# Performance work log

Measured on AMD Instinct MI355X. Metric: run time of the kernel, lower is better.

## Reference

```python
import jax, jax.numpy as jnp
import numpy as np

SIGMA, U = 16.0, 0.0
B, C, L, H = 4, 2048, 96, 8   # L = n_head windows, H = d_k window width
D = L * H                      # d_model = 768
D_INNER = 3072


def make_gauss_mask():
    # replicates My_EncoderLayer.gauss: guass_2d[j, k] = g[(L-1-j) + k]
    x = jnp.arange(-L, L, dtype=jnp.float32)
    g = jnp.exp(-(x - U) ** 2 / (2.0 * SIGMA ** 2))
    g = g / jnp.max(g)
    idx = (L - 1) - jnp.arange(L)[:, None] + jnp.arange(L)[None, :]
    return g[idx]  # (L, L)


def layer_norm(x, g, b, eps=1e-6):
    m = jnp.mean(x, axis=-1, keepdims=True)
    v = jnp.var(x, axis=-1, keepdims=True)
    return (x - m) / jnp.sqrt(v + eps) * g + b


def setup_inputs() -> dict:
    key = jax.random.key(0)
    ks = jax.random.split(key, 16)
    sH = 1.0 / np.sqrt(H)
    sD = 1.0 / np.sqrt(D)
    sI = 1.0 / np.sqrt(D_INNER)
    n = lambda k, shape, s: jax.random.normal(k, shape, jnp.float32) * s
    return {
        "enc_input": jax.random.normal(ks[0], (B, C, D), jnp.float32),
        "mask": make_gauss_mask(),
        "w_q": n(ks[1], (H,), sH), "b_q": n(ks[2], (), sH),
        "w_k": n(ks[3], (H,), sH), "b_k": n(ks[4], (), sH),
        "w_v": n(ks[5], (H,), sH), "b_v": n(ks[6], (), sH),
        "ln1_g": jnp.ones((D,), jnp.float32), "ln1_b": jnp.zeros((D,), jnp.float32),
        "w1": n(ks[7], (D, D_INNER), sD), "b1": n(ks[8], (D_INNER,), sD),
        "w2": n(ks[9], (D_INNER, D), sI), "b2": n(ks[10], (D,), sI),
        "ln2_g": jnp.ones((D,), jnp.float32), "ln2_b": jnp.zeros((D,), jnp.float32),
    }


def reference(enc_input, mask, w_q, b_q, w_k, b_k, w_v, b_v,
              ln1_g, ln1_b, w1, b1, w2, b2, ln2_g, ln2_b):
    Bn, Cn, Dm = enc_input.shape
    Ln = mask.shape[0]
    Hn = Dm // Ln
    heads = enc_input.reshape(Bn, Cn, Ln, Hn)              # unfold(-1, H, H)
    q = jnp.einsum('bclh,h->bcl', heads, w_q) + b_q        # (B,C,L)
    k = jnp.einsum('bclh,h->bcl', heads, w_k) + b_k
    v = jnp.einsum('bclh,h->bcl', heads, w_v) + b_v
    fm = q[..., :, None] * k[..., None, :]                 # outer product (B,C,L,L)
    nrm = jnp.sqrt(jnp.sum(fm * fm, axis=(2, 3), keepdims=True))  # F.normalize over flat L*L
    fm = fm / jnp.maximum(nrm, 1e-12)
    scores = jnp.sum(fm * mask, axis=-1)                   # gaussian-masked sum -> (B,C,L)
    attn = jax.nn.softmax(scores, axis=-1)
    res = attn * v                                         # (B,C,L)
    x = (res[..., None] + heads).reshape(Bn, Cn, Dm)       # broadcast add residual
    x = layer_norm(x, ln1_g, ln1_b)
    # PositionwiseFeedForward: w2(relu(w1(x))) + residual, then LN
    h = jax.nn.relu(jnp.einsum('bcd,df->bcf', x, w1) + b1)
    y = jnp.einsum('bcf,fd->bcd', h, w2) + b2 + x
    return layer_norm(y, ln2_g, ln2_b)
```

## Files before the change

### kernel.cpp

```cpp
#include <hip/hip_runtime.h>

#define ROWS 8192
#define LW 96
#define HW 8
#define DM 768
#define DI 3072

typedef __bf16 bf16x8 __attribute__((ext_vector_type(8)));
typedef float f32x4 __attribute__((ext_vector_type(4)));
typedef unsigned short u16;
typedef unsigned int u32;

__device__ __forceinline__ u16 bfbits(__bf16 b) {
    return __builtin_bit_cast(u16, b);
}
__device__ __forceinline__ void decomp(float v, u16& hi, u16& lo) {
    __bf16 hb = (__bf16)v;
    float hf = (float)hb;
    __bf16 lb = (__bf16)(v - hf);
    hi = bfbits(hb); lo = bfbits(lb);
}
__device__ __forceinline__ void gload16(const void* g, void* l) {
    __builtin_amdgcn_global_load_lds((const __attribute__((address_space(1))) unsigned int*)g,
                                     (__attribute__((address_space(3))) unsigned int*)l, 16, 0, 0);
}
__device__ __forceinline__ float wred_sum(float v) {
#pragma unroll
    for (int o = 32; o; o >>= 1) v += __shfl_xor(v, o);
    return v;
}
__device__ __forceinline__ float wred_max(float v) {
#pragma unroll
    for (int o = 32; o; o >>= 1) v = fmaxf(v, __shfl_xor(v, o));
    return v;
}

__global__ __launch_bounds__(256) void k_wprep(
    const float* __restrict__ W, u16* __restrict__ Th,
    u16* __restrict__ Tl, int K, int N)
{
    __shared__ float tile[32][33];
    const int tx = threadIdx.x & 31, ty = threadIdx.x >> 5;
    const int k0 = blockIdx.y * 32, n0 = blockIdx.x * 32;
#pragma unroll
    for (int i = 0; i < 32; i += 8)
        tile[ty + i][tx] = W[(size_t)(k0 + ty + i) * N + n0 + tx];
    __syncthreads();
#pragma unroll
    for (int i = 0; i < 32; i += 8) {
        int n = n0 + ty + i, k = k0 + tx;
        u16 h, l;
        decomp(tile[tx][ty + i], h, l);
        Th[(size_t)n * K + k] = h;
        Tl[(size_t)n * K + k] = l;
    }
}

__global__ __launch_bounds__(256) void k_attn_ln1(
    const float* __restrict__ inp, const float* __restrict__ mask,
    const float* __restrict__ wq, const float* __restrict__ bq,
    const float* __restrict__ wk, const float* __restrict__ bk,
    const float* __restrict__ wv, const float* __restrict__ bv,
    const float* __restrict__ g1, const float* __restrict__ be1,
    float* __restrict__ xout, u16* __restrict__ xh)
{
    const int t = threadIdx.x, lane = t & 63, w = t >> 6;
    const int row = blockIdx.x * 4 + w;
    __shared__ float kvS[4][96];
    __shared__ float gS[4][192];

    const float* rp = inp + (size_t)row * DM;

    float xr[8], xr2[8];
    {
        float4 a = ((const float4*)rp)[lane * 2];
        float4 b = ((const float4*)rp)[lane * 2 + 1];
        xr[0]=a.x; xr[1]=a.y; xr[2]=a.z; xr[3]=a.w;
        xr[4]=b.x; xr[5]=b.y; xr[6]=b.z; xr[7]=b.w;
    }
    if (lane < 32) {
        float4 a = ((const float4*)rp)[128 + lane * 2];
        float4 b = ((const float4*)rp)[128 + lane * 2 + 1];
        xr2[0]=a.x; xr2[1]=a.y; xr2[2]=a.z; xr2[3]=a.w;
        xr2[4]=b.x; xr2[5]=b.y; xr2[6]=b.z; xr2[7]=b.w;
    } else {
#pragma unroll
        for (int i = 0; i < 8; i++) xr2[i] = 0.f;
    }

    {
        int m1 = lane;
        gS[w][m1] = mask[95 * LW + m1];
        int m2 = 64 + lane;
        gS[w][m2] = (m2 < 96) ? mask[95 * LW + m2] : mask[(190 - m2) * LW + 95];
        int m3 = 128 + lane;
        if (m3 <= 190) gS[w][m3] = mask[(190 - m3) * LW + 95];
    }

    float q1, k1, v1, q2, k2, v2;
    {
        float aq = 0.f, ak = 0.f, av = 0.f, aq2 = 0.f, ak2 = 0.f, av2 = 0.f;
#pragma unroll
        for (int i = 0; i < 8; i++) {
            float wqi = wq[i], wki = wk[i], wvi = wv[i];
            aq = fmaf(xr[i],  wqi, aq);  ak = fmaf(xr[i],  wki, ak);  av = fmaf(xr[i],  wvi, av);
            aq2 = fmaf(xr2[i], wqi, aq2); ak2 = fmaf(xr2[i], wki, ak2); av2 = fmaf(xr2[i], wvi, av2);
        }
        q1 = aq + bq[0]; k1 = ak + bk[0]; v1 = av + bv[0];
        q2 = aq2 + bq[0]; k2 = ak2 + bk[0]; v2 = av2 + bv[0];
    }

    kvS[w][lane] = k1;
    if (lane < 32) kvS[w][64 + lane] = k2;
    asm volatile("s_waitcnt lgkmcnt(0)" ::: "memory");

    float nq2 = wred_sum(q1 * q1 + (lane < 32 ? q2 * q2 : 0.f));
    float nk2 = wred_sum(k1 * k1 + (lane < 32 ? k2 * k2 : 0.f));
    float inv = 1.f / fmaxf(sqrtf(nq2) * sqrtf(nk2), 1e-12f);

    float km1 = 0.f, km2 = 0.f;
    {
        const float* gw = gS[w];
        const float* kw = kvS[w];
        const int b1 = 95 - lane;
        const int b2 = (lane < 32) ? (31 - lane) : 0;
#pragma unroll 4
        for (int kk = 0; kk < 96; kk++) {
            float kv = kw[kk];
            km1 = fmaf(gw[b1 + kk], kv, km1);
            km2 = fmaf(gw[b2 + kk], kv, km2);
        }
    }

    float sc1 = q1 * km1 * inv;
    float sc2 = (lane < 32) ? (q2 * km2 * inv) : -1e30f;
    float mx = wred_max(fmaxf(sc1, sc2));
    float e1 = __expf(sc1 - mx);
    float e2 = (lane < 32) ? __expf(sc2 - mx) : 0.f;
    float se = wred_sum(e1 + e2);
    float r1 = (e1 / se) * v1;
    float r2 = (e2 / se) * v2;

    float xn[8], xn2[8];
    float sum = 0.f;
#pragma unroll
    for (int i = 0; i < 8; i++) { xn[i] = xr[i] + r1; sum += xn[i]; }
    if (lane < 32) {
#pragma unroll
        for (int i = 0; i < 8; i++) { xn2[i] = xr2[i] + r2; sum += xn2[i]; }
    }
    float mean = wred_sum(sum) * (1.f / DM);
    float vs = 0.f;
#pragma unroll
    for (int i = 0; i < 8; i++) { float d = xn[i] - mean; vs += d * d; }
    if (lane < 32) {
#pragma unroll
        for (int i = 0; i < 8; i++) { float d = xn2[i] - mean; vs += d * d; }
    }
    float rstd = rsqrtf(wred_sum(vs) * (1.f / DM) + 1e-6f);

    float* xo = xout + (size_t)row * DM;
    u16* xho = xh + (size_t)row * DM;
    {
        const int d0 = lane * 8;
        float4 ga = ((const float4*)(g1 + d0))[0], gb = ((const float4*)(g1 + d0))[1];
        float4 ba = ((const float4*)(be1 + d0))[0], bb = ((const float4*)(be1 + d0))[1];
        float o[8];
        o[0]=(xn[0]-mean)*rstd*ga.x+ba.x; o[1]=(xn[1]-mean)*rstd*ga.y+ba.y;
        o[2]=(xn[2]-mean)*rstd*ga.z+ba.z; o[3]=(xn[3]-mean)*rstd*ga.w+ba.w;
        o[4]=(xn[4]-mean)*rstd*gb.x+bb.x; o[5]=(xn[5]-mean)*rstd*gb.y+bb.y;
        o[6]=(xn[6]-mean)*rstd*gb.z+bb.z; o[7]=(xn[7]-mean)*rstd*gb.w+bb.w;
        ((float4*)(xo + d0))[0] = make_float4(o[0], o[1], o[2], o[3]);
        ((float4*)(xo + d0))[1] = make_float4(o[4], o[5], o[6], o[7]);
        uint4 pk;
        pk.x = (u32)bfbits((__bf16)o[0]) | ((u32)bfbits((__bf16)o[1]) << 16);
        pk.y = (u32)bfbits((__bf16)o[2]) | ((u32)bfbits((__bf16)o[3]) << 16);
        pk.z = (u32)bfbits((__bf16)o[4]) | ((u32)bfbits((__bf16)o[5]) << 16);
        pk.w = (u32)bfbits((__bf16)o[6]) | ((u32)bfbits((__bf16)o[7]) << 16);
        *(uint4*)(xho + d0) = pk;
    }
    if (lane < 32) {
        const int d0 = 512 + lane * 8;
        float4 ga = ((const float4*)(g1 + d0))[0], gb = ((const float4*)(g1 + d0))[1];
        float4 ba = ((const float4*)(be1 + d0))[0], bb = ((const float4*)(be1 + d0))[1];
        float o[8];
        o[0]=(xn2[0]-mean)*rstd*ga.x+ba.x; o[1]=(xn2[1]-mean)*rstd*ga.y+ba.y;
        o[2]=(xn2[2]-mean)*rstd*ga.z+ba.z; o[3]=(xn2[3]-mean)*rstd*ga.w+ba.w;
        o[4]=(xn2[4]-mean)*rstd*gb.x+bb.x; o[5]=(xn2[5]-mean)*rstd*gb.y+bb.y;
        o[6]=(xn2[6]-mean)*rstd*gb.z+bb.z; o[7]=(xn2[7]-mean)*rstd*gb.w+bb.w;
        ((float4*)(xo + d0))[0] = make_float4(o[0], o[1], o[2], o[3]);
        ((float4*)(xo + d0))[1] = make_float4(o[4], o[5], o[6], o[7]);
        uint4 pk;
        pk.x = (u32)bfbits((__bf16)o[0]) | ((u32)bfbits((__bf16)o[1]) << 16);
        pk.y = (u32)bfbits((__bf16)o[2]) | ((u32)bfbits((__bf16)o[3]) << 16);
        pk.z = (u32)bfbits((__bf16)o[4]) | ((u32)bfbits((__bf16)o[5]) << 16);
        pk.w = (u32)bfbits((__bf16)o[6]) | ((u32)bfbits((__bf16)o[7]) << 16);
        *(uint4*)(xho + d0) = pk;
    }
}

template<int SPLITK, int RELU, int OUT_MODE>
__global__ __launch_bounds__(256, 3) void k_gemm4(
    const u16* __restrict__ Ah,
    const u16* __restrict__ Bh, const u16* __restrict__ Bl,
    const float* __restrict__ bias, float* __restrict__ Cf,
    u16* __restrict__ Ch, int M, int N, int K)
{
    __shared__ u16 S[2 * 12288];

    const int t = threadIdx.x;
    const int lane = t & 63, w = t >> 6;
    const int wm = w >> 1, wn = w & 1;
    const int fr = lane & 15, fq = lane >> 4;

    const int gn = gridDim.x, gm = gridDim.y;
    int Lidx = blockIdx.x + gn * (blockIdx.y + gm * blockIdx.z);
    const int nb = gn * gm * SPLITK;
    int sID = ((nb & 7) == 0) ? ((Lidx & 7) * (nb >> 3) + (Lidx >> 3)) : Lidx;
    const int bz = sID / (gn * gm);
    const int rr = sID - bz * (gn * gm);
    const int bm = rr / gn;
    const int bn = rr - bm * gn;

    const int KS = K / SPLITK;
    const int NT = KS / 32;
    const int kb = bz * KS;

    const int r0 = t >> 2;
    const int c0 = (t & 3) ^ ((r0 >> 1) & 3);
    const size_t aoff  = (size_t)(bm * 128 + r0) * K + kb + c0 * 8;
    const size_t aoff2 = aoff + (size_t)64 * K;
    const size_t boff  = (size_t)(bn * 128 + r0) * K + kb + c0 * 8;
    const size_t boff2 = boff + (size_t)64 * K;
    const int w512 = w * 512;

    f32x4 acc[4][4];
#pragma unroll
    for (int i = 0; i < 4; i++)
#pragma unroll
        for (int j = 0; j < 4; j++) acc[i][j] = (f32x4)0.f;

    int ai[4], bi[4];
#pragma unroll
    for (int i = 0; i < 4; i++) { int rA = wm * 64 + i * 16 + fr; ai[i] = rA * 32 + (fq ^ ((rA >> 1) & 3)) * 8; }
#pragma unroll
    for (int j = 0; j < 4; j++) { int rB = wn * 64 + j * 16 + fr; bi[j] = rB * 32 + (fq ^ ((rB >> 1) & 3)) * 8; }

#define STAGE(tile, bb)                                                  \
    { u16* Lb = S + (bb) * 12288 + w512;                                 \
      const size_t kk = (size_t)(tile) * 32;                             \
      gload16(Ah + aoff  + kk, Lb + 0);                                  \
      gload16(Ah + aoff2 + kk, Lb + 2048);                               \
      gload16(Bh + boff  + kk, Lb + 4096);                               \
      gload16(Bh + boff2 + kk, Lb + 6144);                               \
      gload16(Bl + boff  + kk, Lb + 8192);                               \
      gload16(Bl + boff2 + kk, Lb + 10240); }

#define MM(ii, jj, AA, BH, BL)                                                            \
    acc[ii][jj] = __builtin_amdgcn_mfma_f32_16x16x32_bf16(AA, BH, acc[ii][jj], 0, 0, 0);  \
    acc[ii][jj] = __builtin_amdgcn_mfma_f32_16x16x32_bf16(AA, BL, acc[ii][jj], 0, 0, 0);

    STAGE(0, 0);

    for (int tt = 0; tt < NT; ++tt) {
        if (tt + 1 < NT) {
            STAGE(tt + 1, (tt + 1) & 1);
            asm volatile("s_waitcnt vmcnt(6)" ::: "memory");
        } else {
            asm volatile("s_waitcnt vmcnt(0)" ::: "memory");
        }
        __builtin_amdgcn_s_barrier();

        const u16* Lp = S + (tt & 1) * 12288;
        bf16x8 a[4], bh[4], bl[4];
#pragma unroll
        for (int j = 0; j < 4; j++) {
            bh[j] = *(const bf16x8*)&Lp[4096 + bi[j]];
            bl[j] = *(const bf16x8*)&Lp[8192 + bi[j]];
        }
#pragma unroll
        for (int i = 0; i < 4; i++) a[i] = *(const bf16x8*)&Lp[ai[i]];

        __builtin_amdgcn_s_setprio(1);
#pragma unroll
        for (int j = 0; j < 4; j++)
#pragma unroll
            for (int i = 0; i < 4; i++) { MM(i, j, a[i], bh[j], bl[j]) }
        __builtin_amdgcn_s_setprio(0);

        __builtin_amdgcn_s_barrier();
    }
#undef STAGE
#undef MM

    float* Cp = (OUT_MODE == 1) ? (Cf + (size_t)bz * M * N) : Cf;
#pragma unroll
    for (int i = 0; i < 4; i++) {
        const int row = bm * 128 + wm * 64 + i * 16 + fq * 4;
#pragma unroll
        for (int j = 0; j < 4; j++) {
            const int col = bn * 128 + wn * 64 + j * 16 + fr;
            if (OUT_MODE == 0) {
                const float bb = bias[col];
#pragma unroll
                for (int rg = 0; rg < 4; rg++) {
                    size_t off = (size_t)(row + rg) * N + col;
                    float v = acc[i][j][rg] + bb;
                    if (RELU) v = fmaxf(v, 0.f);
                    Ch[off] = bfbits((__bf16)v);
                }
            } else {
#pragma unroll
                for (int rg = 0; rg < 4; rg++) {
                    size_t off = (size_t)(row + rg) * N + col;
                    Cp[off] = acc[i][j][rg];
                }
            }
        }
    }
}

__global__ __launch_bounds__(256) void k_ln2f(
    const float* __restrict__ y0, const float* __restrict__ y1,
    const float* __restrict__ x, const float* __restrict__ b2,
    const float* __restrict__ g, const float* __restrict__ b,
    float* __restrict__ out)
{
    const int t = threadIdx.x, lane = t & 63, w = t >> 6;
    const int row = blockIdx.x * 4 + w;
    const size_t base = (size_t)row * DM + lane * 12;

    float xs[12]; float sum = 0.f;
#pragma unroll
    for (int i = 0; i < 3; i++) {
        float4 a = ((const float4*)(y0 + base))[i];
        float4 bv = ((const float4*)(y1 + base))[i];
        float4 c = ((const float4*)(x + base))[i];
        float4 d = ((const float4*)(b2 + lane * 12))[i];
        xs[i*4+0] = a.x + bv.x + c.x + d.x;
        xs[i*4+1] = a.y + bv.y + c.y + d.y;
        xs[i*4+2] = a.z + bv.z + c.z + d.z;
        xs[i*4+3] = a.w + bv.w + c.w + d.w;
        sum += xs[i*4+0] + xs[i*4+1] + xs[i*4+2] + xs[i*4+3];
    }
    float mean = wred_sum(sum) * (1.f / DM);
    float vs = 0.f;
#pragma unroll
    for (int i = 0; i < 12; i++) { float dd = xs[i] - mean; vs += dd * dd; }
    float rstd = rsqrtf(wred_sum(vs) * (1.f / DM) + 1e-6f);
#pragma unroll
    for (int i = 0; i < 3; i++) {
        float4 gv = ((const float4*)(g + lane * 12))[i];
        float4 bb = ((const float4*)(b + lane * 12))[i];
        float4 o;
        o.x = (xs[i*4+0] - mean) * rstd * gv.x + bb.x;
        o.y = (xs[i*4+1] - mean) * rstd * gv.y + bb.y;
        o.z = (xs[i*4+2] - mean) * rstd * gv.z + bb.z;
        o.w = (xs[i*4+3] - mean) * rstd * gv.w + bb.w;
        ((float4*)(out + base))[i] = o;
    }
}

extern "C" void kernel_launch(void* const* d_in, const int* in_sizes, int n_in,
                              void* d_out, int out_size, void* d_ws, size_t ws_size,
                              hipStream_t stream) {
    const float* enc  = (const float*)d_in[0];
    const float* mask = (const float*)d_in[1];
    const float* wq = (const float*)d_in[2];  const float* bq = (const float*)d_in[3];
    const float* wk = (const float*)d_in[4];  const float* bk = (const float*)d_in[5];
    const float* wv = (const float*)d_in[6];  const float* bv = (const float*)d_in[7];
    const float* g1 = (const float*)d_in[8];  const float* be1 = (const float*)d_in[9];
    const float* w1 = (const float*)d_in[10]; const float* b1  = (const float*)d_in[11];
    const float* w2 = (const float*)d_in[12]; const float* b2  = (const float*)d_in[13];
    const float* g2 = (const float*)d_in[14]; const float* be2 = (const float*)d_in[15];
    float* out = (float*)d_out;

    char* p = (char*)d_ws;
    float* x  = (float*)p;                 p += (size_t)ROWS * DM * 4;
    float* y01 = (float*)p;                p += 2 * (size_t)ROWS * DM * 4;
    u16* xh = (u16*)p; p += (size_t)ROWS * DM * 2;
    u16* hh = (u16*)p; p += (size_t)ROWS * DI * 2;
    u16* w1h = (u16*)p; p += (size_t)DM * DI * 2;
    u16* w1l = (u16*)p; p += (size_t)DM * DI * 2;
    u16* w2h = (u16*)p; p += (size_t)DM * DI * 2;
    u16* w2l = (u16*)p; p += (size_t)DM * DI * 2;

    k_wprep<<<dim3(DI / 32, DM / 32), 256, 0, stream>>>(w1, w1h, w1l, DM, DI);
    k_wprep<<<dim3(DM / 32, DI / 32), 256, 0, stream>>>(w2, w2h, w2l, DI, DM);

    k_attn_ln1<<<ROWS / 4, 256, 0, stream>>>(enc, mask, wq, bq, wk, bk, wv, bv, g1, be1,
                                             x, xh);

    k_gemm4<1, 1, 0><<<dim3(DI / 128, ROWS / 128, 1), 256, 0, stream>>>(
        xh, w1h, w1l, b1, nullptr, hh, ROWS, DI, DM);

    k_gemm4<2, 0, 1><<<dim3(DM / 128, ROWS / 128, 2), 256, 0, stream>>>(
        hh, w2h, w2l, nullptr, y01, nullptr, ROWS, DM, DI);

    k_ln2f<<<ROWS / 4, 256, 0, stream>>>(y01, y01 + (size_t)ROWS * DM, x, b2, g2, be2, out);
}
```

Before: 316.2 us.

## Switch GEMMs from split bf16 hi/lo weights to single fp16 MFMA

The bf16 hi+lo weight decomposition, which needed two MFMAs per tile and twice the B-operand loads, is replaced by one fp16 copy of each weight and a single fp16 MFMA. Activations are also stored as fp16. LDS per block shrinks, so the occupancy hint goes from 3 to 4 blocks. A block-index remap that walks M fastest is added for the first GEMM. This halves matrix-core work and weight traffic, at the cost of fp16 precision on weights, which risks accuracy loss or overflow for large activations.

After: 255.7 us. 19.2% less time.

```diff
diff --git a/kernel.cpp b/kernel.cpp
--- a/kernel.cpp
+++ b/kernel.cpp
@@ -6,19 +6,15 @@
 #define DM 768
 #define DI 3072
 
-typedef __bf16 bf16x8 __attribute__((ext_vector_type(8)));
+typedef _Float16 f16;
+typedef f16 f16x8 __attribute__((ext_vector_type(8)));
 typedef float f32x4 __attribute__((ext_vector_type(4)));
 typedef unsigned short u16;
 typedef unsigned int u32;
 
-__device__ __forceinline__ u16 bfbits(__bf16 b) {
-    return __builtin_bit_cast(u16, b);
-}
-__device__ __forceinline__ void decomp(float v, u16& hi, u16& lo) {
-    __bf16 hb = (__bf16)v;
-    float hf = (float)hb;
-    __bf16 lb = (__bf16)(v - hf);
-    hi = bfbits(hb); lo = bfbits(lb);
+__device__ __forceinline__ u16 f16bits(float v) {
+    f16 h = (f16)v;
+    return __builtin_bit_cast(u16, h);
 }
 __device__ __forceinline__ void gload16(const void* g, void* l) {
     __builtin_amdgcn_global_load_lds((const __attribute__((address_space(1))) unsigned int*)g,
@@ -36,8 +32,7 @@
 }
 
 __global__ __launch_bounds__(256) void k_wprep(
-    const float* __restrict__ W, u16* __restrict__ Th,
-    u16* __restrict__ Tl, int K, int N)
+    const float* __restrict__ W, u16* __restrict__ Th, int K, int N)
 {
     __shared__ float tile[32][33];
     const int tx = threadIdx.x & 31, ty = threadIdx.x >> 5;
@@ -49,10 +44,7 @@
 #pragma unroll
     for (int i = 0; i < 32; i += 8) {
         int n = n0 + ty + i, k = k0 + tx;
-        u16 h, l;
-        decomp(tile[tx][ty + i], h, l);
-        Th[(size_t)n * K + k] = h;
-        Tl[(size_t)n * K + k] = l;
+        Th[(size_t)n * K + k] = f16bits(tile[tx][ty + i]);
     }
 }
 
@@ -173,10 +165,10 @@
         ((float4*)(xo + d0))[0] = make_float4(o[0], o[1], o[2], o[3]);
         ((float4*)(xo + d0))[1] = make_float4(o[4], o[5], o[6], o[7]);
         uint4 pk;
-        pk.x = (u32)bfbits((__bf16)o[0]) | ((u32)bfbits((__bf16)o[1]) << 16);
-        pk.y = (u32)bfbits((__bf16)o[2]) | ((u32)bfbits((__bf16)o[3]) << 16);
-        pk.z = (u32)bfbits((__bf16)o[4]) | ((u32)bfbits((__bf16)o[5]) << 16);
-        pk.w = (u32)bfbits((__bf16)o[6]) | ((u32)bfbits((__bf16)o[7]) << 16);
+        pk.x = (u32)f16bits(o[0]) | ((u32)f16bits(o[1]) << 16);
+        pk.y = (u32)f16bits(o[2]) | ((u32)f16bits(o[3]) << 16);
+        pk.z = (u32)f16bits(o[4]) | ((u32)f16bits(o[5]) << 16);
+        pk.w = (u32)f16bits(o[6]) | ((u32)f16bits(o[7]) << 16);
         *(uint4*)(xho + d0) = pk;
     }
     if (lane < 32) {
@@ -191,22 +183,21 @@
         ((float4*)(xo + d0))[0] = make_float4(o[0], o[1], o[2], o[3]);
         ((float4*)(xo + d0))[1] = make_float4(o[4], o[5], o[6], o[7]);
         uint4 pk;
-        pk.x = (u32)bfbits((__bf16)o[0]) | ((u32)bfbits((__bf16)o[1]) << 16);
-        pk.y = (u32)bfbits((__bf16)o[2]) | ((u32)bfbits((__bf16)o[3]) << 16);
-        pk.z = (u32)bfbits((__bf16)o[4]) | ((u32)bfbits((__bf16)o[5]) << 16);
-        pk.w = (u32)bfbits((__bf16)o[6]) | ((u32)bfbits((__bf16)o[7]) << 16);
+        pk.x = (u32)f16bits(o[0]) | ((u32)f16bits(o[1]) << 16);
+        pk.y = (u32)f16bits(o[2]) | ((u32)f16bits(o[3]) << 16);
+        pk.z = (u32)f16bits(o[4]) | ((u32)f16bits(o[5]) << 16);
+        pk.w = (u32)f16bits(o[6]) | ((u32)f16bits(o[7]) << 16);
         *(uint4*)(xho + d0) = pk;
     }
 }
 
-template<int SPLITK, int RELU, int OUT_MODE>
-__global__ __launch_bounds__(256, 3) void k_gemm4(
-    const u16* __restrict__ Ah,
-    const u16* __restrict__ Bh, const u16* __restrict__ Bl,
+template<int SPLITK, int RELU, int OUT_MODE, int BMFAST>
+__global__ __launch_bounds__(256, 4) void k_gemm4(
+    const u16* __restrict__ Ah, const u16* __restrict__ Bh,
     const float* __restrict__ bias, float* __restrict__ Cf,
     u16* __restrict__ Ch, int M, int N, int K)
 {
-    __shared__ u16 S[2 * 12288];
+    __shared__ u16 S[2 * 8192];
 
     const int t = threadIdx.x;
     const int lane = t & 63, w = t >> 6;
@@ -219,8 +210,9 @@
     int sID = ((nb & 7) == 0) ? ((Lidx & 7) * (nb >> 3) + (Lidx >> 3)) : Lidx;
     const int bz = sID / (gn * gm);
     const int rr = sID - bz * (gn * gm);
-    const int bm = rr / gn;
-    const int bn = rr - bm * gn;
+    int bm, bn;
+    if (BMFAST) { bm = rr % gm; bn = rr / gm; }
+    else        { bm = rr / gn; bn = rr - (rr / gn) * gn; }
 
     const int KS = K / SPLITK;
     const int NT = KS / 32;
@@ -247,51 +239,42 @@
     for (int j = 0; j < 4; j++) { int rB = wn * 64 + j * 16 + fr; bi[j] = rB * 32 + (fq ^ ((rB >> 1) & 3)) * 8; }
 
 #define STAGE(tile, bb)                                                  \
-    { u16* Lb = S + (bb) * 12288 + w512;                                 \
+    { u16* Lb = S + (bb) * 8192 + w512;                                  \
       const size_t kk = (size_t)(tile) * 32;                             \
       gload16(Ah + aoff  + kk, Lb + 0);                                  \
       gload16(Ah + aoff2 + kk, Lb + 2048);                               \
       gload16(Bh + boff  + kk, Lb + 4096);                               \
-      gload16(Bh + boff2 + kk, Lb + 6144);                               \
-      gload16(Bl + boff  + kk, Lb + 8192);                               \
-      gload16(Bl + boff2 + kk, Lb + 10240); }
-
-#define MM(ii, jj, AA, BH, BL)                                                            \
-    acc[ii][jj] = __builtin_amdgcn_mfma_f32_16x16x32_bf16(AA, BH, acc[ii][jj], 0, 0, 0);  \
-    acc[ii][jj] = __builtin_amdgcn_mfma_f32_16x16x32_bf16(AA, BL, acc[ii][jj], 0, 0, 0);
+      gload16(Bh + boff2 + kk, Lb + 6144); }
 
     STAGE(0, 0);
 
     for (int tt = 0; tt < NT; ++tt) {
         if (tt + 1 < NT) {
             STAGE(tt + 1, (tt + 1) & 1);
-            asm volatile("s_waitcnt vmcnt(6)" ::: "memory");
+            asm volatile("s_waitcnt vmcnt(4)" ::: "memory");
         } else {
             asm volatile("s_waitcnt vmcnt(0)" ::: "memory");
         }
         __builtin_amdgcn_s_barrier();
 
-        const u16* Lp = S + (tt & 1) * 12288;
-        bf16x8 a[4], bh[4], bl[4];
-#pragma unroll
-        for (int j = 0; j < 4; j++) {
-            bh[j] = *(const bf16x8*)&Lp[4096 + bi[j]];
-            bl[j] = *(const bf16x8*)&Lp[8192 + bi[j]];
-        }
-#pragma unroll
-        for (int i = 0; i < 4; i++) a[i] = *(const bf16x8*)&Lp[ai[i]];
+        const u16* Lp = S + (tt & 1) * 8192;
+        f16x8 a[4], b[4];
+#pragma unroll
+        for (int j = 0; j < 4; j++) b[j] = *(const f16x8*)&Lp[4096 + bi[j]];
+#pragma unroll
+        for (int i = 0; i < 4; i++) a[i] = *(const f16x8*)&Lp[ai[i]];
 
         __builtin_amdgcn_s_setprio(1);
 #pragma unroll
         for (int j = 0; j < 4; j++)
 #pragma unroll
-            for (int i = 0; i < 4; i++) { MM(i, j, a[i], bh[j], bl[j]) }
+            for (int i = 0; i < 4; i++)
+                acc[i][j] = __builtin_amdgcn_mfma_f32_16x16x32_f16(a[i], b[j], acc[i][j], 0, 0, 0);
         __builtin_amdgcn_s_setprio(0);
 
         __builtin_amdgcn_s_barrier();
     }
 #undef STAGE
-#undef MM
 
     float* Cp = (OUT_MODE == 1) ? (Cf + (size_t)bz * M * N) : Cf;
 #pragma unroll
@@ -307,7 +290,7 @@
                     size_t off = (size_t)(row + rg) * N + col;
                     float v = acc[i][j][rg] + bb;
                     if (RELU) v = fmaxf(v, 0.f);
-                    Ch[off] = bfbits((__bf16)v);
+                    Ch[off] = f16bits(v);
                 }
             } else {
 #pragma unroll
@@ -381,21 +364,19 @@
     u16* xh = (u16*)p; p += (size_t)ROWS * DM * 2;
     u16* hh = (u16*)p; p += (size_t)ROWS * DI * 2;
     u16* w1h = (u16*)p; p += (size_t)DM * DI * 2;
-    u16* w1l = (u16*)p; p += (size_t)DM * DI * 2;
     u16* w2h = (u16*)p; p += (size_t)DM * DI * 2;
-    u16* w2l = (u16*)p; p += (size_t)DM * DI * 2;
-
-    k_wprep<<<dim3(DI / 32, DM / 32), 256, 0, stream>>>(w1, w1h, w1l, DM, DI);
-    k_wprep<<<dim3(DM / 32, DI / 32), 256, 0, stream>>>(w2, w2h, w2l, DI, DM);
+
+    k_wprep<<<dim3(DI / 32, DM / 32), 256, 0, stream>>>(w1, w1h, DM, DI);
+    k_wprep<<<dim3(DM / 32, DI / 32), 256, 0, stream>>>(w2, w2h, DI, DM);
 
     k_attn_ln1<<<ROWS / 4, 256, 0, stream>>>(enc, mask, wq, bq, wk, bk, wv, bv, g1, be1,
                                              x, xh);
 
-    k_gemm4<1, 1, 0><<<dim3(DI / 128, ROWS / 128, 1), 256, 0, stream>>>(
-        xh, w1h, w1l, b1, nullptr, hh, ROWS, DI, DM);
-
-    k_gemm4<2, 0, 1><<<dim3(DM / 128, ROWS / 128, 2), 256, 0, stream>>>(
-        hh, w2h, w2l, nullptr, y01, nullptr, ROWS, DM, DI);
+    k_gemm4<1, 1, 0, 1><<<dim3(DI / 128, ROWS / 128, 1), 256, 0, stream>>>(
+        xh, w1h, b1, nullptr, hh, ROWS, DI, DM);
+
+    k_gemm4<2, 0, 1, 0><<<dim3(DM / 128, ROWS / 128, 2), 256, 0, stream>>>(
+        hh, w2h, nullptr, y01, nullptr, ROWS, DM, DI);
 
     k_ln2f<<<ROWS / 4, 256, 0, stream>>>(y01, y01 + (size_t)ROWS * DM, x, b2, g2, be2, out);
 }
```
